# Optimization experiments

Hardware: AMD Instinct MI355X
Metric: run time of the kernel (lower is better)

## Reference

```python
import jax
import jax.numpy as jnp
from jax import lax
import numpy as np

N_COLORS = 256  # n_possible_colors; classifier emits N_COLORS+1 logits (last = 'new color')
LRELU_SLOPE = 0.01  # torch nn.LeakyReLU default negative_slope


def setup_inputs() -> dict:
    key = jax.random.key(0)
    ks = jax.random.split(key, 8)
    N, E = 8192, 512
    deg = 32
    s1 = 1.0 / np.sqrt(2 * E)
    s2 = 1.0 / np.sqrt(E)
    s3 = 1.0 / np.sqrt(400)
    return {
        "embeddings": jax.random.normal(ks[0], (N, E), jnp.float32),
        "neighbors": jax.random.randint(ks[1], (N, deg), 0, N, jnp.int32),
        "W1": jax.random.normal(ks[2], (2 * E, E), jnp.float32) * s1,
        "b1": jnp.zeros((E,), jnp.float32),
        "W2": jax.random.normal(ks[3], (E, 400), jnp.float32) * s2,
        "b2": jnp.zeros((400,), jnp.float32),
        "W3": jax.random.normal(ks[4], (400, N_COLORS + 1), jnp.float32) * s3,
        "b3": jnp.zeros((N_COLORS + 1,), jnp.float32),
        "baseline": jnp.ones((), jnp.float32),
    }


def _leaky(x):
    return jnp.where(x >= 0, x, LRELU_SLOPE * x)


def reference(embeddings, neighbors, W1, b1, W2, b2, W3, b3, baseline):
    N, E = embeddings.shape
    C = N_COLORS + 1  # 257 output classes
    graph_emb = embeddings.mean(axis=0)  # torch.mean(embeddings, dim=0), constant across steps
    idx = jnp.arange(C)
    colors0 = jnp.full((N,), -1, jnp.int32).at[0].set(0)  # _assign_color(0, vertex_order[0])
    key0 = jax.random.key(42)

    def step(carry, v):
        colors, n_used, logp, key = carry
        key, sk = jax.random.split(key)
        # classifier MLP: cat(node_emb, graph_emb) -> 512 -> 400 -> 257
        x = jnp.concatenate([embeddings[v], graph_emb])  # [2E]
        h = _leaky(x @ W1 + b1)
        h = _leaky(h @ W2 + b2)
        logits = h @ W3 + b3  # [257]
        # _mask_irrelevant_colors: disable unused colors in [n_used, 256)
        irrel = (idx >= n_used) & (idx < N_COLORS)
        # _mask_colors: disable colors of already-colored neighbors (-1 = uncolored -> padded out)
        nb_c = colors[neighbors[v]]  # [deg]
        adj_mask = jnp.zeros((C + 1,), bool).at[jnp.where(nb_c < 0, C, nb_c)].set(True)[:C]
        logits = jnp.where(irrel | adj_mask, -jnp.inf, logits)
        probs = jax.nn.softmax(logits)  # classifier output
        raw = jax.random.categorical(sk, logits)  # np.random.choice(p=probs)
        chosen = jnp.where(raw == N_COLORS, n_used, raw).astype(jnp.int32)
        n_used = jnp.where(raw == N_COLORS, n_used + 1, n_used)
        colors = colors.at[v].set(chosen)
        p = probs[raw]
        logp = logp + jnp.log(p + 1e-8) - jnp.log(jnp.asarray(1e-8, p.dtype))
        return (colors, n_used, logp, key), None

    init = (colors0, jnp.int32(1), jnp.float32(0.0), key0)
    (colors, n_used, logp, _), _ = lax.scan(step, init, jnp.arange(1, N))
    loss = (n_used.astype(jnp.float32) - baseline) * logp / N
    return colors, loss
```

## Files before the change

### kernel.cpp

```cpp
#include <hip/hip_runtime.h>
#include <stdint.h>
#include <math.h>

#define NV 8192
#define EMB 512
#define CLS 257
#define DEG 32
#define TV 8
#define RSTRIDE 260

struct KP { uint32_t a, b; };

__host__ __device__ constexpr KP tfc(uint32_t k0, uint32_t k1,
                                     uint32_t x0, uint32_t x1) {
  const uint32_t ks2 = k0 ^ k1 ^ 0x1BD11BDAu;
  uint32_t v0 = x0 + k0, v1 = x1 + k1;
#define QR(r) { v0 += v1; v1 = (v1 << (r)) | (v1 >> (32 - (r))); v1 ^= v0; }
  QR(13) QR(15) QR(26) QR(6)
  v0 += k1;  v1 += ks2 + 1u;
  QR(17) QR(29) QR(16) QR(24)
  v0 += ks2; v1 += k0 + 2u;
  QR(13) QR(15) QR(26) QR(6)
  v0 += k0;  v1 += k1 + 3u;
  QR(17) QR(29) QR(16) QR(24)
  v0 += k1;  v1 += ks2 + 4u;
  QR(13) QR(15) QR(26) QR(6)
  v0 += ks2; v1 += k0 + 5u;
#undef QR
  return KP{v0, v1};
}

struct Seg { KP e[256]; };
constexpr Seg mkseg(KP s) {
  Seg g{};
  g.e[0] = s;
  for (int i = 1; i < 256; ++i) g.e[i] = tfc(g.e[i - 1].a, g.e[i - 1].b, 0u, 0u);
  return g;
}
#define NXTSEG(prev) mkseg(tfc(prev.e[255].a, prev.e[255].b, 0u, 0u))
constexpr Seg SG0 = mkseg(KP{0u, 42u});
constexpr Seg SG1 = NXTSEG(SG0);   constexpr Seg SG2 = NXTSEG(SG1);
constexpr Seg SG3 = NXTSEG(SG2);   constexpr Seg SG4 = NXTSEG(SG3);
constexpr Seg SG5 = NXTSEG(SG4);   constexpr Seg SG6 = NXTSEG(SG5);
constexpr Seg SG7 = NXTSEG(SG6);   constexpr Seg SG8 = NXTSEG(SG7);
constexpr Seg SG9 = NXTSEG(SG8);   constexpr Seg SG10 = NXTSEG(SG9);
constexpr Seg SG11 = NXTSEG(SG10); constexpr Seg SG12 = NXTSEG(SG11);
constexpr Seg SG13 = NXTSEG(SG12); constexpr Seg SG14 = NXTSEG(SG13);
constexpr Seg SG15 = NXTSEG(SG14); constexpr Seg SG16 = NXTSEG(SG15);
constexpr Seg SG17 = NXTSEG(SG16); constexpr Seg SG18 = NXTSEG(SG17);
constexpr Seg SG19 = NXTSEG(SG18); constexpr Seg SG20 = NXTSEG(SG19);
constexpr Seg SG21 = NXTSEG(SG20); constexpr Seg SG22 = NXTSEG(SG21);
constexpr Seg SG23 = NXTSEG(SG22); constexpr Seg SG24 = NXTSEG(SG23);
constexpr Seg SG25 = NXTSEG(SG24); constexpr Seg SG26 = NXTSEG(SG25);
constexpr Seg SG27 = NXTSEG(SG26); constexpr Seg SG28 = NXTSEG(SG27);
constexpr Seg SG29 = NXTSEG(SG28); constexpr Seg SG30 = NXTSEG(SG29);
constexpr Seg SG31 = NXTSEG(SG30);

struct KT { uint32_t hi[8192]; uint32_t lo[8192]; };
constexpr KT mkkt() {
  KT t{};
  const Seg* sg[32] = {
    &SG0,  &SG1,  &SG2,  &SG3,  &SG4,  &SG5,  &SG6,  &SG7,
    &SG8,  &SG9,  &SG10, &SG11, &SG12, &SG13, &SG14, &SG15,
    &SG16, &SG17, &SG18, &SG19, &SG20, &SG21, &SG22, &SG23,
    &SG24, &SG25, &SG26, &SG27, &SG28, &SG29, &SG30, &SG31 };
  for (int s = 0; s < 32; ++s)
    for (int i = 0; i < 256; ++i) {
      const int v = 1 + s * 256 + i;
      if (v < 8192) { t.hi[v] = sg[s]->e[i].a; t.lo[v] = sg[s]->e[i].b; }
    }
  return t;
}
__device__ const KT KEYS = mkkt();

__global__ __launch_bounds__(256) void colmean_part(const float* __restrict__ emb,
                                                    float* __restrict__ part) {
  const int b = blockIdx.x;
  const int t = threadIdx.x;
  for (int j = t; j < EMB; j += 256) {
    float s = 0.f;
    const int r0 = b * 128;
    for (int r = 0; r < 128; ++r) s += emb[(size_t)(r0 + r) * EMB + j];
    part[(size_t)b * EMB + j] = s;
  }
}

__global__ __launch_bounds__(256) void colmean_fin(const float* __restrict__ part,
                                                   float* __restrict__ g) {
  const int t = threadIdx.x;
  for (int j = t; j < EMB; j += 256) {
    float s = 0.f;
    for (int b = 0; b < 64; ++b) s += part[(size_t)b * EMB + j];
    g[j] = s / 8192.0f;
  }
}

__global__ __launch_bounds__(256) void mlp3i(
    const float* __restrict__ emb, const float* __restrict__ g,
    const float* __restrict__ W1, const float* __restrict__ b1,
    const float* __restrict__ W2, const float* __restrict__ b2,
    const float* __restrict__ W3, const float* __restrict__ b3,
    float* __restrict__ pl, float* __restrict__ er)
{
  __shared__ float xs[TV][68];
  __shared__ float gs[EMB];
  __shared__ float h1s[TV][EMB];
  __shared__ float h2s[TV][400];
  __shared__ float redw[TV][4];
  __shared__ float li256s[TV];
  __shared__ float mrs[TV];

  const int t  = threadIdx.x;
  const int v0 = blockIdx.x * TV;
  const int j2 = 2 * t;

  for (int j = t; j < EMB; j += 256) gs[j] = g[j];

  float accA[TV], accB[TV];
#pragma unroll
  for (int vv = 0; vv < TV; ++vv) { accA[vv] = 0.f; accB[vv] = 0.f; }

  for (int kc = 0; kc < 8; ++kc) {
    __syncthreads();
    if (t < 128) {
      const int vv = t >> 4;
      const int kk = (t & 15) << 2;
      const float4 s4 = *reinterpret_cast<const float4*>(
          &emb[(size_t)(v0 + vv) * EMB + kc * 64 + kk]);
      xs[vv][kk] = s4.x; xs[vv][kk + 1] = s4.y;
      xs[vv][kk + 2] = s4.z; xs[vv][kk + 3] = s4.w;
    }
    __syncthreads();
    float cA[TV], cB[TV];
#pragma unroll
    for (int vv = 0; vv < TV; ++vv) { cA[vv] = 0.f; cB[vv] = 0.f; }
    for (int q = 0; q < 16; ++q) {
      const int k = kc * 64 + q * 4;
      float2 w[4];
#pragma unroll
      for (int u = 0; u < 4; ++u)
        w[u] = *reinterpret_cast<const float2*>(&W1[(size_t)(k + u) * EMB + j2]);
      float4 xv[TV];
#pragma unroll
      for (int vv = 0; vv < TV; ++vv)
        xv[vv] = *reinterpret_cast<const float4*>(&xs[vv][q * 4]);
#pragma unroll
      for (int u = 0; u < 4; ++u) {
#pragma unroll
        for (int vv = 0; vv < TV; ++vv) {
          const float x = (u == 0) ? xv[vv].x : (u == 1) ? xv[vv].y
                         : (u == 2) ? xv[vv].z : xv[vv].w;
          cA[vv] = fmaf(x, w[u].x, cA[vv]);
          cB[vv] = fmaf(x, w[u].y, cB[vv]);
        }
      }
    }
#pragma unroll
    for (int vv = 0; vv < TV; ++vv) { accA[vv] += cA[vv]; accB[vv] += cB[vv]; }
  }

  float gA = 0.f, gB = 0.f;
  for (int kc = 0; kc < 8; ++kc) {
    float cgA = 0.f, cgB = 0.f;
    for (int q = 0; q < 16; ++q) {
      const int k = kc * 64 + q * 4;
      const float4 gv = *reinterpret_cast<const float4*>(&gs[k]);
      float2 w[4];
#pragma unroll
      for (int u = 0; u < 4; ++u)
        w[u] = *reinterpret_cast<const float2*>(
            &W1[(size_t)(EMB + k + u) * EMB + j2]);
      cgA = fmaf(gv.x, w[0].x, cgA); cgB = fmaf(gv.x, w[0].y, cgB);
      cgA = fmaf(gv.y, w[1].x, cgA); cgB = fmaf(gv.y, w[1].y, cgB);
      cgA = fmaf(gv.z, w[2].x, cgA); cgB = fmaf(gv.z, w[2].y, cgB);
      cgA = fmaf(gv.w, w[3].x, cgA); cgB = fmaf(gv.w, w[3].y, cgB);
    }
    gA += cgA; gB += cgB;
  }

  {
    const float bA = b1[j2], bB = b1[j2 + 1];
#pragma unroll
    for (int vv = 0; vv < TV; ++vv) {
      float hA = (accA[vv] + gA) + bA;
      float hB = (accB[vv] + gB) + bB;
      hA = (hA >= 0.f) ? hA : 0.01f * hA;
      hB = (hB >= 0.f) ? hB : 0.01f * hB;
      *reinterpret_cast<float2*>(&h1s[vv][j2]) = float2{hA, hB};
    }
  }
  __syncthreads();

  if (t < 200) {
    float a2A[TV], a2B[TV];
#pragma unroll
    for (int vv = 0; vv < TV; ++vv) { a2A[vv] = 0.f; a2B[vv] = 0.f; }
    for (int kc = 0; kc < 8; ++kc) {
      float cA[TV], cB[TV];
#pragma unroll
      for (int vv = 0; vv < TV; ++vv) { cA[vv] = 0.f; cB[vv] = 0.f; }
      for (int q = 0; q < 16; ++q) {
        const int k = kc * 64 + q * 4;
        float2 w[4];
#pragma unroll
        for (int u = 0; u < 4; ++u)
          w[u] = *reinterpret_cast<const float2*>(&W2[(size_t)(k + u) * 400 + j2]);
        float4 hv[TV];
#pragma unroll
        for (int vv = 0; vv < TV; ++vv)
          hv[vv] = *reinterpret_cast<const float4*>(&h1s[vv][k]);
#pragma unroll
        for (int u = 0; u < 4; ++u) {
#pragma unroll
          for (int vv = 0; vv < TV; ++vv) {
            const float x = (u == 0) ? hv[vv].x : (u == 1) ? hv[vv].y
                           : (u == 2) ? hv[vv].z : hv[vv].w;
            cA[vv] = fmaf(x, w[u].x, cA[vv]);
            cB[vv] = fmaf(x, w[u].y, cB[vv]);
          }
        }
      }
#pragma unroll
      for (int vv = 0; vv < TV; ++vv) { a2A[vv] += cA[vv]; a2B[vv] += cB[vv]; }
    }
    const float bA = b2[j2], bB = b2[j2 + 1];
#pragma unroll
    for (int vv = 0; vv < TV; ++vv) {
      float hA = a2A[vv] + bA;
      float hB = a2B[vv] + bB;
      hA = (hA >= 0.f) ? hA : 0.01f * hA;
      hB = (hB >= 0.f) ? hB : 0.01f * hB;
      *reinterpret_cast<float2*>(&h2s[vv][j2]) = float2{hA, hB};
    }
  }
  __syncthreads();

  float a3[TV], a3x[TV];
#pragma unroll
  for (int vv = 0; vv < TV; ++vv) { a3[vv] = 0.f; a3x[vv] = 0.f; }
  for (int kc = 0; kc < 8; ++kc) {
    float c3[TV], c3x[TV];
#pragma unroll
    for (int vv = 0; vv < TV; ++vv) { c3[vv] = 0.f; c3x[vv] = 0.f; }
    for (int kk = 0; kk < 50; ++kk) {
      const int k = kc * 50 + kk;
      const float w0 = W3[(size_t)k * CLS + t];
      const float wx = (t == 0) ? W3[(size_t)k * CLS + 256] : 0.f;
#pragma unroll
      for (int vv = 0; vv < TV; ++vv) {
        const float hv = h2s[vv][k];
        c3[vv]  = fmaf(hv, w0, c3[vv]);
        c3x[vv] = fmaf(hv, wx, c3x[vv]);
      }
    }
#pragma unroll
    for (int vv = 0; vv < TV; ++vv) { a3[vv] += c3[vv]; a3x[vv] += c3x[vv]; }
  }

  const float bj = b3[t];
  float li_[TV];
#pragma unroll
  for (int vv = 0; vv < TV; ++vv) li_[vv] = a3[vv] + bj;

#pragma unroll
  for (int vv = 0; vv < TV; ++vv) {
    float m = li_[vv];
#pragma unroll
    for (int off = 1; off < 64; off <<= 1) m = fmaxf(m, __shfl_xor(m, off));
    if ((t & 63) == 0) redw[vv][t >> 6] = m;
  }
  if (t == 0) {
    const float bx = b3[256];
#pragma unroll
    for (int vv = 0; vv < TV; ++vv) li256s[vv] = a3x[vv] + bx;
  }
  __syncthreads();
  if (t < TV) {
    const float m = fmaxf(fmaxf(redw[t][0], redw[t][1]),
                          fmaxf(redw[t][2], redw[t][3]));
    mrs[t] = fmaxf(m, li256s[t]);
  }
  __syncthreads();

#pragma unroll
  for (int vv = 0; vv < TV; ++vv) {
    const int v = v0 + vv;
    const float li = li_[vv];
    const KP sk = tfc(KEYS.hi[v], KEYS.lo[v], 0u, 1u);
    const KP o  = tfc(sk.a, sk.b, 0u, (uint32_t)t);
    const uint32_t bb = o.a ^ o.b;
    const float f = __uint_as_float(0x3f800000u | (bb >> 9)) - 1.0f;
    const float u = fmaxf(1.17549435e-38f, f);
    const float gg = -logf(-logf(u));
    pl[(size_t)v * RSTRIDE + t] = li + gg;
    er[(size_t)v * RSTRIDE + t] = expf(li - mrs[vv]);
  }
  if (t == 0) {
    const float bx = b3[256];
#pragma unroll
    for (int vv = 0; vv < TV; ++vv) {
      const int v = v0 + vv;
      const float li = a3x[vv] + bx;
      const KP sk = tfc(KEYS.hi[v], KEYS.lo[v], 0u, 1u);
      const KP o  = tfc(sk.a, sk.b, 0u, 256u);
      const uint32_t bb = o.a ^ o.b;
      const float f = __uint_as_float(0x3f800000u | (bb >> 9)) - 1.0f;
      const float u = fmaxf(1.17549435e-38f, f);
      const float gg = -logf(-logf(u));
      pl[(size_t)v * RSTRIDE + 256] = li + gg;
      er[(size_t)v * RSTRIDE + 256] = expf(li - mrs[vv]);
    }
  }
}

#define DPPF(CTRL, OLDI, X) \
  __builtin_amdgcn_update_dpp((int)(OLDI), (X), (CTRL), 0xF, 0xF, false)
#define SRED(CTRL) { S += __int_as_float(DPPF(CTRL, 0, __float_as_int(S))); }

__device__ __forceinline__ uint32_t ordmap(float f) {
  const uint32_t s = __float_as_uint(f);
  return s ^ (0x80000000u | (uint32_t)((int32_t)s >> 31));
}

#define WG_SCOPE __HIP_MEMORY_SCOPE_WORKGROUP

__global__ __launch_bounds__(256) void sortrows(float* __restrict__ plbuf) {
  __shared__ uint64_t keys[4][512];
  const int t = threadIdx.x;
  const int w = t >> 6;
  const int lane = t & 63;
  const int v = blockIdx.x * 4 + w;
  const float* row = plbuf + (size_t)v * RSTRIDE;

#pragma unroll
  for (int j = 0; j < 8; ++j) {
    const int i = lane + 64 * j;
    uint32_t om = 0u;
    if (i < CLS) om = ordmap(row[i]);
    keys[w][i] = ((uint64_t)om << 9) | (uint64_t)(511 - i);
  }
  __syncthreads();

  for (int k = 2; k <= 512; k <<= 1) {
    for (int j = k >> 1; j > 0; j >>= 1) {
#pragma unroll
      for (int m = 0; m < 4; ++m) {
        const int p  = lane + 64 * m;
        const int i  = ((p & ~(j - 1)) << 1) | (p & (j - 1));
        const int ix = i | j;
        const uint64_t a = keys[w][i], b = keys[w][ix];
        const bool sw = ((i & k) == 0) ? (a < b) : (a > b);
        if (sw) { keys[w][i] = b; keys[w][ix] = a; }
      }
      __syncthreads();
    }
  }

  uint16_t* o16 = reinterpret_cast<uint16_t*>(plbuf) + (size_t)v * (RSTRIDE * 2);
#pragma unroll
  for (int j = 0; j < 5; ++j) {
    const int i = lane + 64 * j;
    if (i < 320) o16[i] = (uint16_t)(511u - (uint32_t)(keys[w][i] & 511u));
  }
}

__global__ __launch_bounds__(128) void scan8(
    const int* __restrict__ nbrG, const uint32_t* __restrict__ scG,
    unsigned* __restrict__ rawnu, float* __restrict__ out)
{
  __shared__ int colors[NV];
  __shared__ uint32_t scR[32][160];
  __shared__ int nbrRing[1024];
  __shared__ unsigned bbuf[2][16];
  __shared__ int prod_done, cons_done;

  const int t = threadIdx.x;
  const int lane = t & 63;
  const int ln32 = lane & 31;
  const uint16_t* scR16 = reinterpret_cast<const uint16_t*>(&scR[0][0]);

  for (int i = t; i < NV; i += 128) colors[i] = -1;
  if (t == 0) { colors[0] = 0; prod_done = 0; cons_done = 0; }
  __syncthreads();

  if (t >= 64) {
    for (int pc = 0; pc < 1024; ++pc) {
      while (__hip_atomic_load(&cons_done, __ATOMIC_ACQUIRE, WG_SCOPE) < pc - 3)
        __builtin_amdgcn_s_sleep(1);
      uint32_t x[8], y[8], z[8];
#pragma unroll
      for (int r = 0; r < 8; ++r) {
        const size_t base = (size_t)(pc * 8 + r) * RSTRIDE;
        x[r] = scG[base + lane];
        y[r] = scG[base + 64 + lane];
        z[r] = (lane < 32) ? scG[base + 128 + lane] : 0u;
      }
      const int4 nb4 = *reinterpret_cast<const int4*>(nbrG + pc * 256 + 4 * lane);
#pragma unroll
      for (int r = 0; r < 8; ++r) {
        const int slot = (pc * 8 + r) & 31;
        scR[slot][lane] = x[r];
        scR[slot][64 + lane] = y[r];
        if (lane < 32) scR[slot][128 + lane] = z[r];
      }
      *reinterpret_cast<int4*>(&nbrRing[((pc & 3) << 8) + 4 * lane]) = nb4;
      if (lane == 0)
        __hip_atomic_store(&prod_done, pc + 1, __ATOMIC_RELEASE, WG_SCOPE);
    }
    return;
  }

  while (__hip_atomic_load(&prod_done, __ATOMIC_ACQUIRE, WG_SCOPE) < 2) {}

  int c0, c1;
  bool s0a, s0b, s1a, s1b, hf;
  int nbrn;
  {
    const int nb1 = nbrRing[32 + ln32];
    bbuf[1][lane & 15] = 0u;
    hf = (__ballot(nb1 == 0) != 0ULL);
    const int cg0 = colors[nb1];
    if (cg0 >= 0) atomicOr(&bbuf[1][cg0 >> 5], 1u << (cg0 & 31));
    c0 = scR16[320 + lane];
    c1 = scR16[320 + 64 + lane];
    const unsigned w0 = bbuf[1][c0 >> 5];
    const unsigned w1 = bbuf[1][c1 >> 5];
    const bool f0 = !((w0 >> (c0 & 31)) & 1u);
    const bool f1 = !((w1 >> (c1 & 31)) & 1u);
    s0a = f0 && (c0 < 1 || c0 == 256);
    s0b = f0 && (c0 < 2 || c0 == 256);
    s1a = f1 && (c1 < 1 || c1 == 256);
    s1b = f1 && (c1 < 2 || c1 == 256);
    nbrn = nbrRing[64 + ln32];
  }

  int chosen_prev = 0;
  int n_used = 1;
  bool inP = false;

  for (int v = 1; v < NV; ++v) {
    const int vp1 = (v + 1 < NV) ? v + 1 : NV - 1;
    const int vp2 = (v + 2 < NV) ? v + 2 : NV - 1;

    if ((v & 7) == 7) {
      if (lane == 0)
        __hip_atomic_store(&cons_done, (v + 1) >> 3, __ATOMIC_RELEASE, WG_SCOPE);
      int tgt = ((v + 1) >> 3) + 2;
      tgt = tgt > 1024 ? 1024 : tgt;
      while (__hip_atomic_load(&prod_done, __ATOMIC_ACQUIRE, WG_SCOPE) < tgt) {}
    }

    const int sB = (vp1 & 31) * 320;
    const int n0 = scR16[sB + lane];
    const int n1 = scR16[sB + 64 + lane];
    const int nbrn2 = nbrRing[(((vp2 >> 3) & 3) << 8) + ((vp2 & 7) << 5) + ln32];

    const int nb = vp1 & 1;
    bbuf[nb][lane & 15] = 0u;
    const bool hfn = (__ballot(nbrn == v) != 0ULL);
    const int cgn = colors[nbrn];
    if (cgn >= 0) atomicOr(&bbuf[nb][cgn >> 5], 1u << (cgn & 31));
    const unsigned wn0 = bbuf[nb][n0 >> 5];
    const unsigned wn1 = bbuf[nb][n1 >> 5];
    const int nuP = n_used;
    const bool fn0 = !((wn0 >> (n0 & 31)) & 1u);
    const bool fn1 = !((wn1 >> (n1 & 31)) & 1u);
    const bool sn0a = fn0 && (n0 < nuP || n0 == 256);
    const bool sn0b = fn0 && (n0 < nuP + 1 || n0 == 256);
    const bool sn1a = fn1 && (n1 < nuP || n1 == 256);
    const bool sn1b = fn1 && (n1 < nuP + 1 || n1 == 256);

    const int fixc = chosen_prev;
    int raw = 256;
    {
      const bool ok0 = (inP ? s0b : s0a) && !(hf && c0 == fixc);
      uint64_t b_ = __ballot(ok0);
      if (b_) {
        raw = __builtin_amdgcn_readlane(c0, (int)__builtin_ctzll(b_));
      } else {
        const bool ok1 = (inP ? s1b : s1a) && !(hf && c1 == fixc);
        b_ = __ballot(ok1);
        if (b_) {
          raw = __builtin_amdgcn_readlane(c1, (int)__builtin_ctzll(b_));
        } else {
          const int sBv = (v & 31) * 320;
          const int nu = n_used;
          const int x2 = scR16[sBv + 128 + lane];
          const int x3 = scR16[sBv + 192 + lane];
          const int x4 = scR16[sBv + 256 + lane];
          const unsigned q2 = bbuf[v & 1][x2 >> 5];
          const unsigned q3 = bbuf[v & 1][x3 >> 5];
          const unsigned q4 = bbuf[v & 1][x4 >> 5];
          const bool o2 = (!((q2 >> (x2 & 31)) & 1u)) &&
                          (x2 < nu || x2 == 256) && !(hf && x2 == fixc);
          const bool o3 = (!((q3 >> (x3 & 31)) & 1u)) &&
                          (x3 < nu || x3 == 256) && !(hf && x3 == fixc);
          const bool o4 = (!((q4 >> (x4 & 31)) & 1u)) &&
                          (x4 < nu || x4 == 256) && !(hf && x4 == fixc);
          if ((b_ = __ballot(o2)))
            raw = __builtin_amdgcn_readlane(x2, (int)__builtin_ctzll(b_));
          else if ((b_ = __ballot(o3)))
            raw = __builtin_amdgcn_readlane(x3, (int)__builtin_ctzll(b_));
          else if ((b_ = __ballot(o4)))
            raw = __builtin_amdgcn_readlane(x4, (int)__builtin_ctzll(b_));
        }
      }
    }

    const bool isnew = (raw == 256);
    const int chosen = isnew ? n_used : raw;
    if (lane == 0) {
      colors[v] = chosen;
      rawnu[v] = (unsigned)raw | ((unsigned)n_used << 16);
    }
    if (isnew) ++n_used;
    inP = isnew;
    chosen_prev = chosen;

    c0 = n0; c1 = n1;
    s0a = sn0a; s0b = sn0b; s1a = sn1a; s1b = sn1b;
    hf = hfn; nbrn = nbrn2;
  }

  for (int i = lane; i < NV; i += 64) out[i] = (float)colors[i];
}

__global__ __launch_bounds__(256) void logp_part(
    const float* __restrict__ outF, const int* __restrict__ nbrG,
    const float* __restrict__ er, const unsigned* __restrict__ rawnu,
    double* __restrict__ partd)
{
  __shared__ unsigned bb[4][16];
  const int t = threadIdx.x;
  const int w = t >> 6;
  const int lane = t & 63;
  const int ln32 = lane & 31;
  const int b = blockIdx.x;

  double a = 0.0;
  for (int i = 0; i < 32; ++i) {
    const int v = b * 128 + w * 32 + i;
    if (v == 0) continue;
    const unsigned val = rawnu[v];
    const int raw = (int)(val & 0xFFFFu);
    const int nu  = (int)(val >> 16);

    bb[w][lane & 15] = 0u;
    const int u = nbrG[(size_t)v * DEG + ln32];
    const int cu = (u < v) ? (int)outF[u] : -1;
    if (cu >= 0) atomicOr(&bb[w][cu >> 5], 1u << (cu & 31));
    unsigned bwp[4];
#pragma unroll
    for (int j = 0; j < 4; ++j) bwp[j] = bb[w][(lane >> 5) + 2 * j];
    const unsigned bw8 = bb[w][8];

    const size_t base = (size_t)v * RSTRIDE;
    bool mk[4];
    float e[4];
#pragma unroll
    for (int j = 0; j < 4; ++j) {
      const int c = lane + 64 * j;
      mk[j] = (((bwp[j] >> ln32) & 1u) != 0u) || (c >= nu);
      e[j] = mk[j] ? 0.f : er[base + c];
    }
    const bool mkX = ((bw8 & 1u) != 0u);
    const float eX = er[base + 256];
    const float e4 = (!mkX && lane == 0) ? eX : 0.f;

    float S = ((e[0] + e[1]) + (e[2] + e[3])) + e4;
    SRED(0x111) SRED(0x112) SRED(0x114) SRED(0x118) SRED(0x142) SRED(0x143)
    const float Sall = __int_as_float(
        __builtin_amdgcn_readlane(__float_as_int(S), 63));

    const bool isnew = (raw == 256);
    const int jsel  = isnew ? 4 : (raw >> 6);
    const int owner = isnew ? 0 : (raw & 63);
    const float cand = (jsel == 0) ? e[0] : (jsel == 1) ? e[1]
                     : (jsel == 2) ? e[2] : (jsel == 3) ? e[3] : e4;
    const float praw = __int_as_float(
        __builtin_amdgcn_readlane(__float_as_int(cand), owner));

    const float p = praw / Sall;
    a += (double)(logf(p + 1e-8f) - logf(1e-8f));
  }
  if (lane == 0) partd[b * 4 + w] = a;
}

__global__ __launch_bounds__(64) void finalize(
    const double* __restrict__ partd, const unsigned* __restrict__ rawnu,
    const float* __restrict__ baseline, float* __restrict__ out)
{
  if (threadIdx.x == 0) {
    double lp = 0.0;
    for (int i = 0; i < 256; ++i) lp += partd[i];
    const unsigned val = rawnu[NV - 1];
    const unsigned nf = (val >> 16) + (((val & 0xFFFFu) == 256u) ? 1u : 0u);
    out[NV] = ((float)nf - baseline[0]) * (float)lp / 8192.0f;
  }
}

extern "C" void kernel_launch(void* const* d_in, const int* in_sizes, int n_in,
                              void* d_out, int out_size, void* d_ws, size_t ws_size,
                              hipStream_t stream) {
  const float* emb      = (const float*)d_in[0];
  const int*   nbr      = (const int*)d_in[1];
  const float* W1       = (const float*)d_in[2];
  const float* b1       = (const float*)d_in[3];
  const float* W2       = (const float*)d_in[4];
  const float* b2       = (const float*)d_in[5];
  const float* W3       = (const float*)d_in[6];
  const float* b3       = (const float*)d_in[7];
  const float* baseline = (const float*)d_in[8];
  float* out = (float*)d_out;

  char* ws = (char*)d_ws;
  float* g     = (float*)ws;
  float* plbuf = (float*)(ws + 2048);
  float* erbuf = (float*)(ws + 2048 + NV * RSTRIDE * 4);
  float* part  = erbuf;
  unsigned* rawnu = (unsigned*)(ws + 2048);
  double*   partd = (double*)(ws + 2048 + 65536);

  colmean_part<<<64, 256, 0, stream>>>(emb, part);
  colmean_fin<<<1, 256, 0, stream>>>(part, g);
  mlp3i<<<NV / TV, 256, 0, stream>>>(emb, g, W1, b1, W2, b2, W3, b3, plbuf, erbuf);
  sortrows<<<NV / 4, 256, 0, stream>>>(plbuf);
  scan8<<<1, 128, 0, stream>>>(nbr, (const uint32_t*)plbuf, rawnu, out);
  logp_part<<<64, 256, 0, stream>>>((const float*)out, nbr, erbuf, rawnu, partd);
  finalize<<<1, 64, 0, stream>>>(partd, rawnu, baseline, out);
}
```

Measured before the change: 3.024 ms.

## Deepen software pipeline in serial coloring scan and merge top-candidate ballots

Restructures the single-wavefront sequential coloring loop so neighbor-color gathering and bitmask building for step v+1 happen one step further ahead, loading candidate words as packed 32-bit pairs. The first two candidates are checked with one combined ballot instead of two. The inP-dependent dual predicates are dropped because eligibility for the next step is computed after n_used is updated. This is meant to shorten the serial per-step dependency chain, at the cost of more live registers and subtle correctness reasoning about the lookahead.

Measured after the change: 2.907 ms. 1.04x faster.

```diff
diff --git a/kernel.cpp b/kernel.cpp
--- a/kernel.cpp
+++ b/kernel.cpp
@@ -364,7 +364,7 @@
   }
 }
 
-__global__ __launch_bounds__(128) void scan8(
+__global__ __launch_bounds__(128) void scan9(
     const int* __restrict__ nbrG, const uint32_t* __restrict__ scG,
     unsigned* __restrict__ rawnu, float* __restrict__ out)
 {
@@ -412,35 +412,95 @@
 
   while (__hip_atomic_load(&prod_done, __ATOMIC_ACQUIRE, WG_SCOPE) < 2) {}
 
-  int c0, c1;
-  bool s0a, s0b, s1a, s1b, hf;
-  int nbrn;
+  int cp1 = 0;
+  int n_used = 1;
+
+  int c0, c1, d0, d1;
+  bool sb0, sb1, hf;
+  int nbrA, nbrB, cgv1;
   {
-    const int nb1 = nbrRing[32 + ln32];
     bbuf[1][lane & 15] = 0u;
-    hf = (__ballot(nb1 == 0) != 0ULL);
-    const int cg0 = colors[nb1];
-    if (cg0 >= 0) atomicOr(&bbuf[1][cg0 >> 5], 1u << (cg0 & 31));
-    c0 = scR16[320 + lane];
-    c1 = scR16[320 + 64 + lane];
+    const int nb1 = nbrRing[(1 << 5) + ln32];
+    const int cg = colors[nb1];
+    if (cg >= 0) atomicOr(&bbuf[1][cg >> 5], 1u << (cg & 31));
+    const uint32_t cw = scR[1][lane];
+    c0 = (int)(cw & 0xFFFFu); c1 = (int)(cw >> 16);
     const unsigned w0 = bbuf[1][c0 >> 5];
     const unsigned w1 = bbuf[1][c1 >> 5];
-    const bool f0 = !((w0 >> (c0 & 31)) & 1u);
-    const bool f1 = !((w1 >> (c1 & 31)) & 1u);
-    s0a = f0 && (c0 < 1 || c0 == 256);
-    s0b = f0 && (c0 < 2 || c0 == 256);
-    s1a = f1 && (c1 < 1 || c1 == 256);
-    s1b = f1 && (c1 < 2 || c1 == 256);
-    nbrn = nbrRing[64 + ln32];
-  }
-
-  int chosen_prev = 0;
-  int n_used = 1;
-  bool inP = false;
+    sb0 = (!((w0 >> (c0 & 31)) & 1u)) && (c0 < 1 || c0 == 256);
+    sb1 = (!((w1 >> (c1 & 31)) & 1u)) && (c1 < 1 || c1 == 256);
+    hf = false;
+    const uint32_t dw = scR[2][lane];
+    d0 = (int)(dw & 0xFFFFu); d1 = (int)(dw >> 16);
+    nbrA = nbrRing[(2 << 5) + ln32];
+    cgv1 = colors[nbrA];
+    nbrB = nbrRing[(3 << 5) + ln32];
+  }
 
   for (int v = 1; v < NV; ++v) {
-    const int vp1 = (v + 1 < NV) ? v + 1 : NV - 1;
+    const int slotN = (v + 1) & 1;
+
+    bbuf[slotN][lane & 15] = 0u;
+    if (cgv1 >= 0) atomicOr(&bbuf[slotN][cgv1 >> 5], 1u << (cgv1 & 31));
+    const unsigned wd0 = bbuf[slotN][d0 >> 5];
+    const unsigned wd1 = bbuf[slotN][d1 >> 5];
+
+    const int nu0 = n_used;
+    const int fixc = cp1;
+    int raw = 256;
+    {
+      const bool okE = sb0 && !(hf && c0 == fixc);
+      const bool okO = sb1 && !(hf && c1 == fixc);
+      uint64_t b_ = __ballot(okE || okO);
+      if (b_) {
+        const int sel = okE ? c0 : c1;
+        raw = __builtin_amdgcn_readlane(sel, (int)__builtin_ctzll(b_));
+      } else {
+        const int sBv = (v & 31) * 320;
+        const int x2 = scR16[sBv + 128 + lane];
+        const int x3 = scR16[sBv + 192 + lane];
+        const int x4 = scR16[sBv + 256 + lane];
+        const unsigned q2 = bbuf[v & 1][x2 >> 5];
+        const unsigned q3 = bbuf[v & 1][x3 >> 5];
+        const unsigned q4 = bbuf[v & 1][x4 >> 5];
+        const bool o2 = (!((q2 >> (x2 & 31)) & 1u)) &&
+                        (x2 < nu0 || x2 == 256) && !(hf && x2 == fixc);
+        const bool o3 = (!((q3 >> (x3 & 31)) & 1u)) &&
+                        (x3 < nu0 || x3 == 256) && !(hf && x3 == fixc);
+        const bool o4 = (!((q4 >> (x4 & 31)) & 1u)) &&
+                        (x4 < nu0 || x4 == 256) && !(hf && x4 == fixc);
+        if ((b_ = __ballot(o2)))
+          raw = __builtin_amdgcn_readlane(x2, (int)__builtin_ctzll(b_));
+        else if ((b_ = __ballot(o3)))
+          raw = __builtin_amdgcn_readlane(x3, (int)__builtin_ctzll(b_));
+        else if ((b_ = __ballot(o4)))
+          raw = __builtin_amdgcn_readlane(x4, (int)__builtin_ctzll(b_));
+      }
+    }
+    const bool isnew = (raw == 256);
+    const int chosen = isnew ? nu0 : raw;
+    if (lane == 0) {
+      colors[v] = chosen;
+      rawnu[v] = (unsigned)raw | ((unsigned)nu0 << 16);
+    }
+    if (isnew) ++n_used;
+    cp1 = chosen;
+
+    const int nuN = n_used;
+    const bool sbn0 = (!((wd0 >> (d0 & 31)) & 1u)) && (d0 < nuN || d0 == 256);
+    const bool sbn1 = (!((wd1 >> (d1 & 31)) & 1u)) && (d1 < nuN || d1 == 256);
+    const bool hfn = (__ballot(nbrA == v) != 0ULL);
+
+    const int cgv2 = colors[nbrB];
+
     const int vp2 = (v + 2 < NV) ? v + 2 : NV - 1;
+    const int vp3 = (v + 3 < NV) ? v + 3 : NV - 1;
+    const uint32_t ew = scR[vp2 & 31][lane];
+    const int nbrC = nbrRing[(((vp3 >> 3) & 3) << 8) + ((vp3 & 7) << 5) + ln32];
+
+    c0 = d0; c1 = d1; sb0 = sbn0; sb1 = sbn1; hf = hfn;
+    d0 = (int)(ew & 0xFFFFu); d1 = (int)(ew >> 16);
+    cgv1 = cgv2; nbrA = nbrB; nbrB = nbrC;
 
     if ((v & 7) == 7) {
       if (lane == 0)
@@ -449,77 +509,6 @@
       tgt = tgt > 1024 ? 1024 : tgt;
       while (__hip_atomic_load(&prod_done, __ATOMIC_ACQUIRE, WG_SCOPE) < tgt) {}
     }
-
-    const int sB = (vp1 & 31) * 320;
-    const int n0 = scR16[sB + lane];
-    const int n1 = scR16[sB + 64 + lane];
-    const int nbrn2 = nbrRing[(((vp2 >> 3) & 3) << 8) + ((vp2 & 7) << 5) + ln32];
-
-    const int nb = vp1 & 1;
-    bbuf[nb][lane & 15] = 0u;
-    const bool hfn = (__ballot(nbrn == v) != 0ULL);
-    const int cgn = colors[nbrn];
-    if (cgn >= 0) atomicOr(&bbuf[nb][cgn >> 5], 1u << (cgn & 31));
-    const unsigned wn0 = bbuf[nb][n0 >> 5];
-    const unsigned wn1 = bbuf[nb][n1 >> 5];
-    const int nuP = n_used;
-    const bool fn0 = !((wn0 >> (n0 & 31)) & 1u);
-    const bool fn1 = !((wn1 >> (n1 & 31)) & 1u);
-    const bool sn0a = fn0 && (n0 < nuP || n0 == 256);
-    const bool sn0b = fn0 && (n0 < nuP + 1 || n0 == 256);
-    const bool sn1a = fn1 && (n1 < nuP || n1 == 256);
-    const bool sn1b = fn1 && (n1 < nuP + 1 || n1 == 256);
-
-    const int fixc = chosen_prev;
-    int raw = 256;
-    {
-      const bool ok0 = (inP ? s0b : s0a) && !(hf && c0 == fixc);
-      uint64_t b_ = __ballot(ok0);
-      if (b_) {
-        raw = __builtin_amdgcn_readlane(c0, (int)__builtin_ctzll(b_));
-      } else {
-        const bool ok1 = (inP ? s1b : s1a) && !(hf && c1 == fixc);
-        b_ = __ballot(ok1);
-        if (b_) {
-          raw = __builtin_amdgcn_readlane(c1, (int)__builtin_ctzll(b_));
-        } else {
-          const int sBv = (v & 31) * 320;
-          const int nu = n_used;
-          const int x2 = scR16[sBv + 128 + lane];
-          const int x3 = scR16[sBv + 192 + lane];
-          const int x4 = scR16[sBv + 256 + lane];
-          const unsigned q2 = bbuf[v & 1][x2 >> 5];
-          const unsigned q3 = bbuf[v & 1][x3 >> 5];
-          const unsigned q4 = bbuf[v & 1][x4 >> 5];
-          const bool o2 = (!((q2 >> (x2 & 31)) & 1u)) &&
-                          (x2 < nu || x2 == 256) && !(hf && x2 == fixc);
-          const bool o3 = (!((q3 >> (x3 & 31)) & 1u)) &&
-                          (x3 < nu || x3 == 256) && !(hf && x3 == fixc);
-          const bool o4 = (!((q4 >> (x4 & 31)) & 1u)) &&
-                          (x4 < nu || x4 == 256) && !(hf && x4 == fixc);
-          if ((b_ = __ballot(o2)))
-            raw = __builtin_amdgcn_readlane(x2, (int)__builtin_ctzll(b_));
-          else if ((b_ = __ballot(o3)))
-            raw = __builtin_amdgcn_readlane(x3, (int)__builtin_ctzll(b_));
-          else if ((b_ = __ballot(o4)))
-            raw = __builtin_amdgcn_readlane(x4, (int)__builtin_ctzll(b_));
-        }
-      }
-    }
-
-    const bool isnew = (raw == 256);
-    const int chosen = isnew ? n_used : raw;
-    if (lane == 0) {
-      colors[v] = chosen;
-      rawnu[v] = (unsigned)raw | ((unsigned)n_used << 16);
-    }
-    if (isnew) ++n_used;
-    inP = isnew;
-    chosen_prev = chosen;
-
-    c0 = n0; c1 = n1;
-    s0a = sn0a; s0b = sn0b; s1a = sn1a; s1b = sn1b;
-    hf = hfn; nbrn = nbrn2;
   }
 
   for (int i = lane; i < NV; i += 64) out[i] = (float)colors[i];
@@ -625,7 +614,7 @@
   colmean_fin<<<1, 256, 0, stream>>>(part, g);
   mlp3i<<<NV / TV, 256, 0, stream>>>(emb, g, W1, b1, W2, b2, W3, b3, plbuf, erbuf);
   sortrows<<<NV / 4, 256, 0, stream>>>(plbuf);
-  scan8<<<1, 128, 0, stream>>>(nbr, (const uint32_t*)plbuf, rawnu, out);
+  scan9<<<1, 128, 0, stream>>>(nbr, (const uint32_t*)plbuf, rawnu, out);
   logp_part<<<64, 256, 0, stream>>>((const float*)out, nbr, erbuf, rawnu, partd);
   finalize<<<1, 64, 0, stream>>>(partd, rawnu, baseline, out);
 }
```
